# Kernel tuning notes

Measured on AMD Instinct MI355X. Metric: run time of the kernel, lower is better.

## Reference

```python
import jax, jax.numpy as jnp
import numpy as np

BETA = 0.25  # commitment/codebook mixing as in VQVAE.__init__


def setup_inputs() -> dict:
    key = jax.random.key(0)
    k1, k2 = jax.random.split(key)
    # z: encoder latent [B, C, H, W] with C = latent_dim
    z = jax.random.normal(k1, (32, 64, 64, 64), dtype=jnp.float32)
    # codebook: nn.Embedding(num_embeddings, latent_dim).weight
    codebook = jax.random.normal(k2, (1024, 64), dtype=jnp.float32)
    return {"z": z, "codebook": codebook}


def reference(z, codebook):
    B, C, H, W = z.shape
    zf = z.reshape(B, C, H * W).transpose(0, 2, 1)  # [B, N, C], N = H*W
    # Squared Euclidean distances; argmin identical to torch.cdist(p=2) argmin
    # since sqrt is monotone (min_distances are unused in the original forward).
    d2 = (jnp.sum(zf * zf, axis=-1, keepdims=True)              # [B, N, 1]
          + jnp.sum(codebook * codebook, axis=-1)[None, None, :]  # [1, 1, K]
          - 2.0 * jnp.einsum('bnc,kc->bnk', zf, codebook))        # [B, N, K]
    indices = jnp.argmin(d2, axis=-1)                            # [B, N]
    z_q = codebook[indices]                                      # [B, N, C] gather
    z_q = z_q.transpose(0, 2, 1).reshape(B, C, H, W)
    commitment_loss = jnp.mean((jax.lax.stop_gradient(z_q) - z) ** 2)
    codebook_loss = jnp.mean((z_q - jax.lax.stop_gradient(z)) ** 2)
    loss = commitment_loss + BETA * codebook_loss
    return z_q, loss
```

## Files before the change

kernel.cpp:

```cpp
#include <hip/hip_runtime.h>
#include <float.h>

#define HW    4096
#define NC    64
#define NK    1024
#define NB    32
#define NPIX  (NB*HW)
#define TOTAL (NPIX*NC)
#define PPB   128

#define MARGIN 8e-3f

typedef __attribute__((ext_vector_type(8))) short short8;
typedef __attribute__((ext_vector_type(4))) float floatx4;

__device__ __forceinline__ unsigned short f2bf(float f) {
    unsigned u = __float_as_uint(f);
    u += 0x7FFFu + ((u >> 16) & 1u);
    return (unsigned short)(u >> 16);
}
__device__ __forceinline__ float bf2f(unsigned short h) {
    return __uint_as_float(((unsigned)h) << 16);
}

__global__ void vq_prep_kernel(const float* __restrict__ cb,
                               float* __restrict__ cnorm,
                               unsigned short* __restrict__ cb_hi,
                               unsigned short* __restrict__ cb_lo,
                               float* __restrict__ loss_out) {
    const int b = blockIdx.x;
    if (b < 64) {
        const int i = b * 256 + threadIdx.x;
        if (i == 0) loss_out[0] = 0.0f;
        float4 v = ((const float4*)cb)[i];
        unsigned short h0 = f2bf(v.x), h1 = f2bf(v.y),
                       h2 = f2bf(v.z), h3 = f2bf(v.w);
        unsigned short l0 = f2bf(v.x - bf2f(h0)), l1 = f2bf(v.y - bf2f(h1)),
                       l2 = f2bf(v.z - bf2f(h2)), l3 = f2bf(v.w - bf2f(h3));
        uint2 ph = make_uint2((unsigned)h0 | ((unsigned)h1 << 16),
                              (unsigned)h2 | ((unsigned)h3 << 16));
        uint2 pl = make_uint2((unsigned)l0 | ((unsigned)l1 << 16),
                              (unsigned)l2 | ((unsigned)l3 << 16));
        ((uint2*)cb_hi)[i] = ph;
        ((uint2*)cb_lo)[i] = pl;
    } else {
        const int k = (b - 64) * 256 + threadIdx.x;
        const float4* r4 = (const float4*)(cb + (size_t)k * NC);
        double s = 0.0;
        #pragma unroll
        for (int j = 0; j < 16; ++j) {
            float4 v = r4[j];
            s = fma((double)v.x, (double)v.x, s);
            s = fma((double)v.y, (double)v.y, s);
            s = fma((double)v.z, (double)v.z, s);
            s = fma((double)v.w, (double)v.w, s);
        }
        cnorm[k] = (float)s;
    }
}

__global__ __launch_bounds__(256, 4) void vq_mfma_kernel(
        const float* __restrict__ z,
        const float* __restrict__ cb,
        const unsigned short* __restrict__ cb_hi,
        const unsigned short* __restrict__ cb_lo,
        const float* __restrict__ cnorm,
        float* __restrict__ zq,
        float* __restrict__ loss_out) {
    __shared__ alignas(16) uint4  abuf[2][1024];
    __shared__ alignas(16) float  cn_lds[NK];
    __shared__ int   finidx[PPB];
    __shared__ int   flags[PPB];
    __shared__ float redf[4];

    const int tid = threadIdx.x;
    const int g0  = blockIdx.x * PPB;
    const int bb  = g0 >> 12;
    const int pp0 = g0 & 4095;
    const float* zbase = z  + (size_t)bb * (NC * HW) + pp0;
    float*      zqbase = zq + (size_t)bb * (NC * HW) + pp0;

    ((float4*)cn_lds)[tid] = ((const float4*)cnorm)[tid];

    const int lane = tid & 63;
    const int w    = tid >> 6;
    const int q    = lane >> 4;
    const int pcol = lane & 15;

    const int  sidx  = tid & 127;
    const int  spart = tid >> 7;
    const int  sswz  = (sidx & ~7) | ((sidx & 7) ^ ((sidx >> 3) & 7));
    const char* gsrc = (spart == 0 ? (const char*)cb_hi : (const char*)cb_lo)
                       + (size_t)sswz * 16;

    auto stage_iv = [&](int iv, int buf) {
        #pragma unroll
        for (int tt = 0; tt < 4; ++tt)
            __builtin_amdgcn_global_load_lds(
                (const __attribute__((address_space(1))) void*)
                    (gsrc + (size_t)iv * 8192 + (size_t)tt * 2048),
                (__attribute__((address_space(3))) void*)
                    &abuf[buf][tt * 256 + tid],
                16, 0, 0);
    };

    stage_iv(0, 0);

    float zraw[2][2][8];
    #pragma unroll
    for (int ks = 0; ks < 2; ++ks)
        #pragma unroll
        for (int j = 0; j < 2; ++j)
            #pragma unroll
            for (int t = 0; t < 8; ++t)
                zraw[ks][j][t] = zbase[(size_t)(ks * 32 + q * 8 + t) * HW
                                       + (w * 32 + j * 16 + pcol)];
    short8 Bh[2][2], Bl[2][2];
    #pragma unroll
    for (int ks = 0; ks < 2; ++ks)
        #pragma unroll
        for (int j = 0; j < 2; ++j)
            #pragma unroll
            for (int t = 0; t < 8; ++t) {
                float v = -2.0f * zraw[ks][j][t];
                unsigned short h = f2bf(v);
                unsigned short l = f2bf(v - bf2f(h));
                Bh[ks][j][t] = (short)h;
                Bl[ks][j][t] = (short)l;
            }

    const int ridx0 = pcol * 8 + (q ^ (pcol & 7));
    const int ridx1 = pcol * 8 + ((4 + q) ^ (pcol & 7));

    __syncthreads();

    float B1[2] = {FLT_MAX, FLT_MAX};
    float B2[2] = {FLT_MAX, FLT_MAX};
    int   I1[2] = {0, 0};

    auto tile_body = [&](short8 ah0, short8 ah1, short8 al0, short8 al1,
                         int tile) {
        const floatx4 cn4 = *(const floatx4*)&cn_lds[tile * 16 + q * 4];
        const int kb = tile * 16 + q * 4;
        #pragma unroll
        for (int j = 0; j < 2; ++j) {
            floatx4 a0 = __builtin_amdgcn_mfma_f32_16x16x32_bf16(ah0, Bh[0][j], cn4, 0, 0, 0);
            floatx4 a1 = {0.f, 0.f, 0.f, 0.f};
            a1 = __builtin_amdgcn_mfma_f32_16x16x32_bf16(ah1, Bh[1][j], a1, 0, 0, 0);
            a0 = __builtin_amdgcn_mfma_f32_16x16x32_bf16(ah0, Bl[0][j], a0, 0, 0, 0);
            a1 = __builtin_amdgcn_mfma_f32_16x16x32_bf16(ah1, Bl[1][j], a1, 0, 0, 0);
            a0 = __builtin_amdgcn_mfma_f32_16x16x32_bf16(al0, Bh[0][j], a0, 0, 0, 0);
            a1 = __builtin_amdgcn_mfma_f32_16x16x32_bf16(al1, Bh[1][j], a1, 0, 0, 0);

            #pragma unroll
            for (int i = 0; i < 4; ++i) {
                float s = a0[i] + a1[i];
                bool lt = s < B1[j];
                I1[j] = lt ? (kb + i) : I1[j];
                B2[j] = __builtin_amdgcn_fmed3f(s, B1[j], B2[j]);
                B1[j] = fminf(s, B1[j]);
            }
        }
    };

    for (int iv = 0; iv < 16; ++iv) {
        if (iv < 15) stage_iv(iv + 1, (iv + 1) & 1);
        const short8* Abase = (const short8*)&abuf[iv & 1][0];
        #pragma unroll
        for (int tt = 0; tt < 4; ++tt) {
            const short8* A = Abase + tt * 256;
            short8 ah0 = A[ridx0];
            short8 ah1 = A[ridx1];
            short8 al0 = A[128 + ridx0];
            short8 al1 = A[128 + ridx1];
            tile_body(ah0, ah1, al0, al1, iv * 4 + tt);
        }
        __syncthreads();
    }

    #pragma unroll
    for (int j = 0; j < 2; ++j) {
        float b1 = B1[j], b2 = B2[j];
        int i1 = I1[j];
        #pragma unroll
        for (int d = 16; d <= 32; d <<= 1) {
            float ob1 = __shfl_xor(b1, d);
            float ob2 = __shfl_xor(b2, d);
            int   oi1 = __shfl_xor(i1, d);
            float nb2 = fminf(fmaxf(b1, ob1), fminf(b2, ob2));
            bool lt = (ob1 < b1) || (ob1 == b1 && oi1 < i1);
            b1 = lt ? ob1 : b1;
            i1 = lt ? oi1 : i1;
            b2 = nb2;
        }
        if (q == 0) {
            const int px = w * 32 + j * 16 + pcol;
            finidx[px] = i1;
            flags[px]  = (b2 - b1 < MARGIN) ? 1 : 0;
        }
    }
    int myflag = 0;
    __syncthreads();
    if (tid < PPB) myflag = flags[tid];
    const int nflag = __syncthreads_count(myflag);

    if (nflag > 0) {
        double* red_s = reinterpret_cast<double*>(cn_lds);
        int*    red_i = reinterpret_cast<int*>(cn_lds + 512);
        for (int p = 0; p < PPB; ++p) {
            if (flags[p]) {
                const float* zp = zbase + p;
                double bd = 1.0e300; int bi = 0;
                #pragma unroll 1
                for (int r = 0; r < 4; ++r) {
                    const int k = tid * 4 + r;
                    const float* rowp = cb + (size_t)k * NC;
                    double s = 0.0;
                    for (int c = 0; c < NC; ++c) {
                        double t = (double)zp[(size_t)c * HW] - (double)rowp[c];
                        s = fma(t, t, s);
                    }
                    if (s < bd) { bd = s; bi = k; }
                }
                red_s[tid] = bd; red_i[tid] = bi;
                __syncthreads();
                if (tid < 64) {
                    double m = red_s[tid]; int mi = red_i[tid];
                    #pragma unroll
                    for (int t = 1; t < 4; ++t) {
                        double om = red_s[tid + 64 * t];
                        int    oi = red_i[tid + 64 * t];
                        if (om < m || (om == m && oi < mi)) { m = om; mi = oi; }
                    }
                    #pragma unroll
                    for (int off = 32; off > 0; off >>= 1) {
                        double om = __shfl_down(m, off);
                        int    oi = __shfl_down(mi, off);
                        if (om < m || (om == m && oi < mi)) { m = om; mi = oi; }
                    }
                    if (tid == 0) finidx[p] = mi;
                }
                __syncthreads();
            }
        }
        __syncthreads();
    }

    {
        const int p  = tid & (PPB - 1);
        const int qq = tid >> 7;
        const int fi = finidx[p];
        const float4* crow4 = (const float4*)(cb + (size_t)fi * NC) + qq * 8;
        float sse = 0.f;
        #pragma unroll
        for (int j = 0; j < 8; ++j) {
            const float4 qv = crow4[j];
            const size_t c0 = (size_t)(qq * 32 + 4 * j) * HW + p;
            const float z0 = zbase[c0];
            const float z1 = zbase[c0 + HW];
            const float z2 = zbase[c0 + 2 * (size_t)HW];
            const float z3 = zbase[c0 + 3 * (size_t)HW];
            zqbase[c0]                  = qv.x;
            zqbase[c0 + HW]             = qv.y;
            zqbase[c0 + 2 * (size_t)HW] = qv.z;
            zqbase[c0 + 3 * (size_t)HW] = qv.w;
            float t0 = qv.x - z0, t1 = qv.y - z1, t2 = qv.z - z2, t3 = qv.w - z3;
            sse = fmaf(t0, t0, sse);
            sse = fmaf(t1, t1, sse);
            sse = fmaf(t2, t2, sse);
            sse = fmaf(t3, t3, sse);
        }
        #pragma unroll
        for (int off = 32; off > 0; off >>= 1) sse += __shfl_down(sse, off);
        if ((tid & 63) == 0) redf[tid >> 6] = sse;
        __syncthreads();
        if (tid == 0)
            atomicAdd(loss_out, (redf[0] + redf[1] + redf[2] + redf[3]) *
                                (1.25f / (float)TOTAL));
    }
}

extern "C" void kernel_launch(void* const* d_in, const int* in_sizes, int n_in,
                              void* d_out, int out_size, void* d_ws, size_t ws_size,
                              hipStream_t stream) {
    const float* z  = (const float*)d_in[0];
    const float* cb = (const float*)d_in[1];
    float* out      = (float*)d_out;
    float* zqp      = out;
    float* loss     = out + TOTAL;

    float* cnorm          = (float*)d_ws;
    unsigned short* cb_hi = (unsigned short*)((char*)d_ws + 4096);
    unsigned short* cb_lo = (unsigned short*)((char*)d_ws + 4096 + NK * NC * 2);

    vq_prep_kernel<<<68, 256, 0, stream>>>(cb, cnorm, cb_hi, cb_lo, loss);
    vq_mfma_kernel<<<NPIX / PPB, 256, 0, stream>>>(z, cb, cb_hi, cb_lo, cnorm,
                                                   zqp, loss);
}
```

Baseline: 173.6 us.

## Split each block's 128 pixels across 8 waves instead of 4

```diff
diff --git a/kernel.cpp b/kernel.cpp
--- a/kernel.cpp
+++ b/kernel.cpp
@@ -59,7 +59,7 @@
     }
 }
 
-__global__ __launch_bounds__(256, 4) void vq_mfma_kernel(
+__global__ __launch_bounds__(512, 8) void vq_mfma_kernel(
         const float* __restrict__ z,
         const float* __restrict__ cb,
         const unsigned short* __restrict__ cb_hi,
@@ -71,7 +71,7 @@
     __shared__ alignas(16) float  cn_lds[NK];
     __shared__ int   finidx[PPB];
     __shared__ int   flags[PPB];
-    __shared__ float redf[4];
+    __shared__ float redf[8];
 
     const int tid = threadIdx.x;
     const int g0  = blockIdx.x * PPB;
@@ -80,88 +80,63 @@
     const float* zbase = z  + (size_t)bb * (NC * HW) + pp0;
     float*      zqbase = zq + (size_t)bb * (NC * HW) + pp0;
 
-    ((float4*)cn_lds)[tid] = ((const float4*)cnorm)[tid];
+    ((float2*)cn_lds)[tid] = ((const float2*)cnorm)[tid];
 
     const int lane = tid & 63;
     const int w    = tid >> 6;
     const int q    = lane >> 4;
     const int pcol = lane & 15;
 
-    const int  sidx  = tid & 127;
-    const int  spart = tid >> 7;
-    const int  sswz  = (sidx & ~7) | ((sidx & 7) ^ ((sidx >> 3) & 7));
-    const char* gsrc = (spart == 0 ? (const char*)cb_hi : (const char*)cb_lo)
-                       + (size_t)sswz * 16;
+    auto src_of = [&](int s) -> const char* {
+        const int tt = s >> 8, part = (s >> 7) & 1;
+        const int row = (s >> 3) & 15, chunk = s & 7;
+        const char* bp = part ? (const char*)cb_lo : (const char*)cb_hi;
+        return bp + tt * 2048 + row * 128 + ((chunk ^ (row & 7)) * 16);
+    };
+    const char* gsrc1 = src_of(tid);
+    const char* gsrc2 = src_of(tid + 512);
 
     auto stage_iv = [&](int iv, int buf) {
-        #pragma unroll
-        for (int tt = 0; tt < 4; ++tt)
-            __builtin_amdgcn_global_load_lds(
-                (const __attribute__((address_space(1))) void*)
-                    (gsrc + (size_t)iv * 8192 + (size_t)tt * 2048),
-                (__attribute__((address_space(3))) void*)
-                    &abuf[buf][tt * 256 + tid],
-                16, 0, 0);
+        __builtin_amdgcn_global_load_lds(
+            (const __attribute__((address_space(1))) void*)
+                (gsrc1 + (size_t)iv * 8192),
+            (__attribute__((address_space(3))) void*)&abuf[buf][tid],
+            16, 0, 0);
+        __builtin_amdgcn_global_load_lds(
+            (const __attribute__((address_space(1))) void*)
+                (gsrc2 + (size_t)iv * 8192),
+            (__attribute__((address_space(3))) void*)&abuf[buf][tid + 512],
+            16, 0, 0);
     };
 
     stage_iv(0, 0);
 
-    float zraw[2][2][8];
+    float zraw[2][8];
     #pragma unroll
     for (int ks = 0; ks < 2; ++ks)
         #pragma unroll
-        for (int j = 0; j < 2; ++j)
-            #pragma unroll
-            for (int t = 0; t < 8; ++t)
-                zraw[ks][j][t] = zbase[(size_t)(ks * 32 + q * 8 + t) * HW
-                                       + (w * 32 + j * 16 + pcol)];
-    short8 Bh[2][2], Bl[2][2];
+        for (int t = 0; t < 8; ++t)
+            zraw[ks][t] = zbase[(size_t)(ks * 32 + q * 8 + t) * HW
+                                + (w * 16 + pcol)];
+    short8 Bh[2], Bl[2];
     #pragma unroll
     for (int ks = 0; ks < 2; ++ks)
         #pragma unroll
-        for (int j = 0; j < 2; ++j)
-            #pragma unroll
-            for (int t = 0; t < 8; ++t) {
-                float v = -2.0f * zraw[ks][j][t];
-                unsigned short h = f2bf(v);
-                unsigned short l = f2bf(v - bf2f(h));
-                Bh[ks][j][t] = (short)h;
-                Bl[ks][j][t] = (short)l;
-            }
+        for (int t = 0; t < 8; ++t) {
+            float v = -2.0f * zraw[ks][t];
+            unsigned short h = f2bf(v);
+            unsigned short l = f2bf(v - bf2f(h));
+            Bh[ks][t] = (short)h;
+            Bl[ks][t] = (short)l;
+        }
 
     const int ridx0 = pcol * 8 + (q ^ (pcol & 7));
     const int ridx1 = pcol * 8 + ((4 + q) ^ (pcol & 7));
 
     __syncthreads();
 
-    float B1[2] = {FLT_MAX, FLT_MAX};
-    float B2[2] = {FLT_MAX, FLT_MAX};
-    int   I1[2] = {0, 0};
-
-    auto tile_body = [&](short8 ah0, short8 ah1, short8 al0, short8 al1,
-                         int tile) {
-        const floatx4 cn4 = *(const floatx4*)&cn_lds[tile * 16 + q * 4];
-        const int kb = tile * 16 + q * 4;
-        #pragma unroll
-        for (int j = 0; j < 2; ++j) {
-            floatx4 a0 = __builtin_amdgcn_mfma_f32_16x16x32_bf16(ah0, Bh[0][j], cn4, 0, 0, 0);
-            floatx4 a1 = {0.f, 0.f, 0.f, 0.f};
-            a1 = __builtin_amdgcn_mfma_f32_16x16x32_bf16(ah1, Bh[1][j], a1, 0, 0, 0);
-            a0 = __builtin_amdgcn_mfma_f32_16x16x32_bf16(ah0, Bl[0][j], a0, 0, 0, 0);
-            a1 = __builtin_amdgcn_mfma_f32_16x16x32_bf16(ah1, Bl[1][j], a1, 0, 0, 0);
-            a0 = __builtin_amdgcn_mfma_f32_16x16x32_bf16(al0, Bh[0][j], a0, 0, 0, 0);
-            a1 = __builtin_amdgcn_mfma_f32_16x16x32_bf16(al1, Bh[1][j], a1, 0, 0, 0);
-
-            #pragma unroll
-            for (int i = 0; i < 4; ++i) {
-                float s = a0[i] + a1[i];
-                bool lt = s < B1[j];
-                I1[j] = lt ? (kb + i) : I1[j];
-                B2[j] = __builtin_amdgcn_fmed3f(s, B1[j], B2[j]);
-                B1[j] = fminf(s, B1[j]);
-            }
-        }
-    };
+    float B1 = FLT_MAX, B2 = FLT_MAX;
+    int   I1 = 0;
 
     for (int iv = 0; iv < 16; ++iv) {
         if (iv < 15) stage_iv(iv + 1, (iv + 1) & 1);
@@ -173,15 +148,32 @@
             short8 ah1 = A[ridx1];
             short8 al0 = A[128 + ridx0];
             short8 al1 = A[128 + ridx1];
-            tile_body(ah0, ah1, al0, al1, iv * 4 + tt);
+            const int tile = iv * 4 + tt;
+            const floatx4 cn4 = *(const floatx4*)&cn_lds[tile * 16 + q * 4];
+            const int kb = tile * 16 + q * 4;
+            floatx4 a0 = __builtin_amdgcn_mfma_f32_16x16x32_bf16(ah0, Bh[0], cn4, 0, 0, 0);
+            floatx4 a1 = {0.f, 0.f, 0.f, 0.f};
+            a1 = __builtin_amdgcn_mfma_f32_16x16x32_bf16(ah1, Bh[1], a1, 0, 0, 0);
+            a0 = __builtin_amdgcn_mfma_f32_16x16x32_bf16(ah0, Bl[0], a0, 0, 0, 0);
+            a1 = __builtin_amdgcn_mfma_f32_16x16x32_bf16(ah1, Bl[1], a1, 0, 0, 0);
+            a0 = __builtin_amdgcn_mfma_f32_16x16x32_bf16(al0, Bh[0], a0, 0, 0, 0);
+            a1 = __builtin_amdgcn_mfma_f32_16x16x32_bf16(al1, Bh[1], a1, 0, 0, 0);
+
+            #pragma unroll
+            for (int i = 0; i < 4; ++i) {
+                float s = a0[i] + a1[i];
+                bool lt = s < B1;
+                I1 = lt ? (kb + i) : I1;
+                B2 = __builtin_amdgcn_fmed3f(s, B1, B2);
+                B1 = fminf(s, B1);
+            }
         }
         __syncthreads();
     }
 
-    #pragma unroll
-    for (int j = 0; j < 2; ++j) {
-        float b1 = B1[j], b2 = B2[j];
-        int i1 = I1[j];
+    {
+        float b1 = B1, b2 = B2;
+        int i1 = I1;
         #pragma unroll
         for (int d = 16; d <= 32; d <<= 1) {
             float ob1 = __shfl_xor(b1, d);
@@ -194,7 +186,7 @@
             b2 = nb2;
         }
         if (q == 0) {
-            const int px = w * 32 + j * 16 + pcol;
+            const int px = w * 16 + pcol;
             finidx[px] = i1;
             flags[px]  = (b2 - b1 < MARGIN) ? 1 : 0;
         }
@@ -206,14 +198,14 @@
 
     if (nflag > 0) {
         double* red_s = reinterpret_cast<double*>(cn_lds);
-        int*    red_i = reinterpret_cast<int*>(cn_lds + 512);
+        int*    red_i = reinterpret_cast<int*>(&abuf[0][0]);
         for (int p = 0; p < PPB; ++p) {
             if (flags[p]) {
                 const float* zp = zbase + p;
                 double bd = 1.0e300; int bi = 0;
                 #pragma unroll 1
-                for (int r = 0; r < 4; ++r) {
-                    const int k = tid * 4 + r;
+                for (int r = 0; r < 2; ++r) {
+                    const int k = tid * 2 + r;
                     const float* rowp = cb + (size_t)k * NC;
                     double s = 0.0;
                     for (int c = 0; c < NC; ++c) {
@@ -227,7 +219,7 @@
                 if (tid < 64) {
                     double m = red_s[tid]; int mi = red_i[tid];
                     #pragma unroll
-                    for (int t = 1; t < 4; ++t) {
+                    for (int t = 1; t < 8; ++t) {
                         double om = red_s[tid + 64 * t];
                         int    oi = red_i[tid + 64 * t];
                         if (om < m || (om == m && oi < mi)) { m = om; mi = oi; }
@@ -250,12 +242,12 @@
         const int p  = tid & (PPB - 1);
         const int qq = tid >> 7;
         const int fi = finidx[p];
-        const float4* crow4 = (const float4*)(cb + (size_t)fi * NC) + qq * 8;
+        const float4* crow4 = (const float4*)(cb + (size_t)fi * NC) + qq * 4;
         float sse = 0.f;
         #pragma unroll
-        for (int j = 0; j < 8; ++j) {
+        for (int j = 0; j < 4; ++j) {
             const float4 qv = crow4[j];
-            const size_t c0 = (size_t)(qq * 32 + 4 * j) * HW + p;
+            const size_t c0 = (size_t)(qq * 16 + 4 * j) * HW + p;
             const float z0 = zbase[c0];
             const float z1 = zbase[c0 + HW];
             const float z2 = zbase[c0 + 2 * (size_t)HW];
@@ -274,9 +266,12 @@
         for (int off = 32; off > 0; off >>= 1) sse += __shfl_down(sse, off);
         if ((tid & 63) == 0) redf[tid >> 6] = sse;
         __syncthreads();
-        if (tid == 0)
-            atomicAdd(loss_out, (redf[0] + redf[1] + redf[2] + redf[3]) *
-                                (1.25f / (float)TOTAL));
+        if (tid == 0) {
+            float tot = 0.f;
+            #pragma unroll
+            for (int r = 0; r < 8; ++r) tot += redf[r];
+            atomicAdd(loss_out, tot * (1.25f / (float)TOTAL));
+        }
     }
 }
 
@@ -294,6 +289,6 @@
     unsigned short* cb_lo = (unsigned short*)((char*)d_ws + 4096 + NK * NC * 2);
 
     vq_prep_kernel<<<68, 256, 0, stream>>>(cb, cnorm, cb_hi, cb_lo, loss);
-    vq_mfma_kernel<<<NPIX / PPB, 256, 0, stream>>>(z, cb, cb_hi, cb_lo, cnorm,
+    vq_mfma_kernel<<<NPIX / PPB, 512, 0, stream>>>(z, cb, cb_hi, cb_lo, cnorm,
                                                    zqp, loss);
 }
```

After: 174.9 us, median of 2. No clear change (+0.7%).
